# Kernel tuning notes

Measured on AMD Instinct MI355X. Metric: run time of the kernel, lower is better.

The kernel has to match this reference:

```python
import jax, jax.numpy as jnp
import numpy as np


def _iterative_pinv(mat, n_iter=6):
    # mat: [b, h, m, m]
    m = mat.shape[-1]
    I = jnp.eye(m, dtype=mat.dtype)
    # global (over all batch/heads) scaling, matching torch.max over full tensor
    init_coef = jnp.max(jnp.sum(jnp.abs(mat), axis=-2)) * jnp.max(jnp.sum(jnp.abs(mat), axis=-1))
    out = jnp.swapaxes(mat, -2, -1) / init_coef
    for _ in range(n_iter):
        mo = jnp.matmul(mat, out)          # [b,h,m,m]
        term1 = 7.0 * I - mo
        term2 = 15.0 * I - jnp.matmul(mo, term1)
        term3 = 13.0 * I - jnp.matmul(mo, term2)
        out = 0.25 * jnp.matmul(out, term3)
    return out


def _landmarks(x, m):
    # x: [b, h, s, d] -> segment means [b, h, m, d]
    b, h, s, d = x.shape
    l = s // m
    return x.reshape(b, h, m, l, d).mean(axis=-2)


def setup_inputs() -> dict:
    key = jax.random.key(0)
    kq, kk, kv = jax.random.split(key, 3)
    shape = (4, 12, 4096, 64)
    return {
        "query": jax.random.normal(kq, shape, dtype=jnp.float32),
        "key": jax.random.normal(kk, shape, dtype=jnp.float32),
        "value": jax.random.normal(kv, shape, dtype=jnp.float32),
        "num_landmarks": 64,
    }


def reference(query, key, value, num_landmarks):
    b, h, s, d = query.shape
    scale = 1.0 / jnp.sqrt(jnp.asarray(d, dtype=query.dtype))
    q_lm = _landmarks(query, num_landmarks)   # [b,h,m,d]
    k_lm = _landmarks(key, num_landmarks)     # [b,h,m,d]
    # F_tilde: [b,h,s,m]
    F_tilde = jax.nn.softmax(jnp.einsum('bhsd,bhmd->bhsm', query, k_lm) * scale, axis=-1)
    # A_tilde: pinv of [b,h,m,m]
    A_tilde = _iterative_pinv(
        jax.nn.softmax(jnp.einsum('bhnd,bhmd->bhnm', q_lm, k_lm) * scale, axis=-1))
    # B_tilde: [b,h,m,s]
    B_tilde = jax.nn.softmax(jnp.einsum('bhmd,bhsd->bhms', q_lm, key) * scale, axis=-1)
    # out = F_tilde @ (A_tilde @ (B_tilde @ value))  -> [b,h,s,d]
    bv = jnp.matmul(B_tilde, value)        # [b,h,m,d]
    abv = jnp.matmul(A_tilde, bv)          # [b,h,m,d]
    return jnp.matmul(F_tilde, abv)        # [b,h,s,d]
```

## Files before the change

### kernel.cpp

```cpp
#include <hip/hip_runtime.h>
#include <math.h>

#define BH 48
#define Ss 4096
#define Dd 64
#define Mm 64
#define NCH 16
#define SCALE 0.125f
#define PLN 4096

typedef unsigned int u32;
typedef unsigned short u16;
typedef __attribute__((ext_vector_type(8))) short short8;
typedef __attribute__((ext_vector_type(4))) float floatx4;

union FRAG { uint4 u; short8 s; };

#define MFMA(a,b,c) __builtin_amdgcn_mfma_f32_16x16x32_bf16(a,b,c,0,0,0)

__device__ __forceinline__ u32 pack2_hi(float a, float b) {
    return (__float_as_uint(a) >> 16) | (__float_as_uint(b) & 0xFFFF0000u);
}
__device__ __forceinline__ float trunc_bf(float a) {
    return __uint_as_float(__float_as_uint(a) & 0xFFFF0000u);
}
__device__ __forceinline__ void split1(float v, u16& h, u16& l) {
    u32 u = __float_as_uint(v);
    h = (u16)(u >> 16);
    float r = v - __uint_as_float(u & 0xFFFF0000u);
    l = (u16)(__float_as_uint(r) >> 16);
}
__device__ __forceinline__ void split8(const float* v, short8& h, short8& l) {
    FRAG H, L;
    float r[8];
#pragma unroll
    for (int i = 0; i < 8; i++) r[i] = v[i] - trunc_bf(v[i]);
    H.u.x = pack2_hi(v[0], v[1]); H.u.y = pack2_hi(v[2], v[3]);
    H.u.z = pack2_hi(v[4], v[5]); H.u.w = pack2_hi(v[6], v[7]);
    L.u.x = pack2_hi(r[0], r[1]); L.u.y = pack2_hi(r[2], r[3]);
    L.u.z = pack2_hi(r[4], r[5]); L.u.w = pack2_hi(r[6], r[7]);
    h = H.s; l = L.s;
}
__device__ __forceinline__ int swz(int row, int col) {
    return row * 64 + ((((col >> 3) ^ (row & 7)) << 3) | (col & 7));
}

__global__ __launch_bounds__(256) void k_landmarks(const float* __restrict__ Q,
                                                   const float* __restrict__ Kg,
                                                   float* __restrict__ qlm,
                                                   float* __restrict__ klm,
                                                   u16* __restrict__ qlmh, u16* __restrict__ qlml,
                                                   u16* __restrict__ klmh, u16* __restrict__ klml) {
    int g = blockIdx.x, bh = blockIdx.y;
    int t = threadIdx.x;
    int m8 = t >> 5, r5 = t & 31, half = r5 >> 4, d4 = r5 & 15;
    int m = g * 8 + m8;
    __shared__ float4 part[8][16];
    const float* src = blockIdx.z ? Kg : Q;
    float* dst = blockIdx.z ? klm : qlm;
    u16* dh = blockIdx.z ? klmh : qlmh;
    u16* dl = blockIdx.z ? klml : qlml;
    const float* base = src + ((size_t)bh * Ss + (size_t)m * 64 + half * 32) * Dd + d4 * 4;
    float4 acc = make_float4(0.f, 0.f, 0.f, 0.f);
#pragma unroll
    for (int l = 0; l < 32; l++) {
        float4 v = *(const float4*)(base + (size_t)l * Dd);
        acc.x += v.x; acc.y += v.y; acc.z += v.z; acc.w += v.w;
    }
    if (half) part[m8][d4] = acc;
    __syncthreads();
    if (!half) {
        float4 o = part[m8][d4];
        acc.x = (acc.x + o.x) * (1.f / 64.f);
        acc.y = (acc.y + o.y) * (1.f / 64.f);
        acc.z = (acc.z + o.z) * (1.f / 64.f);
        acc.w = (acc.w + o.w) * (1.f / 64.f);
        int idx = (bh * Mm + m) * Dd + d4 * 4;
        *(float4*)(dst + idx) = acc;
        float vv[4] = {acc.x, acc.y, acc.z, acc.w};
        u16 hh[4], ll[4];
#pragma unroll
        for (int i = 0; i < 4; i++) split1(vv[i], hh[i], ll[i]);
        *(uint2*)(dh + idx) = make_uint2((u32)hh[0] | ((u32)hh[1] << 16), (u32)hh[2] | ((u32)hh[3] << 16));
        *(uint2*)(dl + idx) = make_uint2((u32)ll[0] | ((u32)ll[1] << 16), (u32)ll[2] | ((u32)ll[3] << 16));
    }
}

__global__ __launch_bounds__(256) void k_lmsm(const float* __restrict__ qlm,
                                              const float* __restrict__ klm,
                                              float* __restrict__ smat,
                                              unsigned int* __restrict__ coef) {
    int bh = blockIdx.x, t = threadIdx.x;
    __shared__ float kl[Mm * Dd];
    __shared__ float ql[Mm * Dd];
    __shared__ float Lp[Mm][Mm + 1];
    const float4* kb = (const float4*)(klm + bh * Mm * Dd);
    const float4* qb = (const float4*)(qlm + bh * Mm * Dd);
    for (int i = t; i < Mm * Dd / 4; i += 256) {
        ((float4*)kl)[i] = kb[i];
        ((float4*)ql)[i] = qb[i];
    }
    __syncthreads();
    int n = t >> 2, c = t & 3;
    float p[16];
#pragma unroll
    for (int jj = 0; jj < 16; jj++) {
        int m = c * 16 + jj;
        float s = 0.f;
#pragma unroll
        for (int d4 = 0; d4 < 16; d4++) {
            int d = (((d4 + c * 4) & 15)) * 4;
            float4 kv = *(const float4*)(kl + m * Dd + d);
            float4 qv = *(const float4*)(ql + n * Dd + d);
            s += qv.x * kv.x + qv.y * kv.y + qv.z * kv.z + qv.w * kv.w;
        }
        p[jj] = s * SCALE;
    }
    float mx = -INFINITY;
#pragma unroll
    for (int jj = 0; jj < 16; jj++) mx = fmaxf(mx, p[jj]);
    mx = fmaxf(mx, __shfl_xor(mx, 1));
    mx = fmaxf(mx, __shfl_xor(mx, 2));
    float den = 0.f;
#pragma unroll
    for (int jj = 0; jj < 16; jj++) { p[jj] = __expf(p[jj] - mx); den += p[jj]; }
    den += __shfl_xor(den, 1);
    den += __shfl_xor(den, 2);
    float inv = 1.0f / den;
#pragma unroll
    for (int jj = 0; jj < 16; jj++) Lp[n][c * 16 + jj] = p[jj] * inv;
    __syncthreads();
    float* sg = smat + bh * Mm * Mm;
    for (int i = t; i < Mm * Mm; i += 256) sg[i] = Lp[i >> 6][i & 63];
    if (t < Mm) {
        float cs = 0.f;
#pragma unroll
        for (int nn = 0; nn < Mm; nn++) cs += Lp[nn][t];
#pragma unroll
        for (int off = 1; off < 64; off <<= 1) cs = fmaxf(cs, __shfl_xor(cs, off));
        if (t == 0) atomicMax(coef + 0, __float_as_uint(cs));
    } else if (t < 2 * Mm) {
        int nn = t - Mm; float rs = 0.f;
#pragma unroll
        for (int m = 0; m < Mm; m++) rs += Lp[nn][m];
#pragma unroll
        for (int off = 1; off < 64; off <<= 1) rs = fmaxf(rs, __shfl_xor(rs, off));
        if (t == Mm) atomicMax(coef + 1, __float_as_uint(rs));
    }
}

__device__ __forceinline__ void pinv_pass(const u16* __restrict__ Ah, const u16* __restrict__ Al,
                                          const u16* __restrict__ Bph, const u16* __restrict__ Bpl,
                                          u16* __restrict__ Oh, u16* __restrict__ Ol,
                                          int w, int c, int hi,
                                          float diag, float sgn, float scl) {
    short8 bfh[2], bfl[2];
#pragma unroll
    for (int ks = 0; ks < 2; ks++) {
        bfh[ks] = *(const short8*)&Bph[swz(w * 16 + c, ks * 32 + hi * 8)];
        bfl[ks] = *(const short8*)&Bpl[swz(w * 16 + c, ks * 32 + hi * 8)];
    }
    int j = w * 16 + c;
#pragma unroll
    for (int ta = 0; ta < 4; ta++) {
        floatx4 acc = (floatx4){0.f, 0.f, 0.f, 0.f};
#pragma unroll
        for (int ks = 0; ks < 2; ks++) {
            short8 afh = *(const short8*)&Ah[swz(ta * 16 + c, ks * 32 + hi * 8)];
            short8 afl = *(const short8*)&Al[swz(ta * 16 + c, ks * 32 + hi * 8)];
            acc = MFMA(afh, bfh[ks], acc);
            acc = MFMA(afl, bfh[ks], acc);
            acc = MFMA(afh, bfl[ks], acc);
        }
        u16 oh[4], ol[4];
#pragma unroll
        for (int r = 0; r < 4; r++) {
            int i = ta * 16 + hi * 4 + r;
            float v = scl * (((i == j) ? diag : 0.f) + sgn * acc[r]);
            split1(v, oh[r], ol[r]);
        }
        int o0 = swz(j, ta * 16 + hi * 4);
        *(u32*)&Oh[o0]     = (u32)oh[0] | ((u32)oh[1] << 16);
        *(u32*)&Oh[o0 + 2] = (u32)oh[2] | ((u32)oh[3] << 16);
        *(u32*)&Ol[o0]     = (u32)ol[0] | ((u32)ol[1] << 16);
        *(u32*)&Ol[o0 + 2] = (u32)ol[2] | ((u32)ol[3] << 16);
    }
}

__global__ __launch_bounds__(256) void k_pinv(const float* __restrict__ smat,
                                              const unsigned int* __restrict__ coef,
                                              float* __restrict__ atil) {
    extern __shared__ u16 P[];
    u16* FaH  = P;             u16* FaL  = P + PLN;
    u16* FxcH = P + 2 * PLN;   u16* FxcL = P + 3 * PLN;
    u16* X0H  = P + 4 * PLN;   u16* X0L  = P + 5 * PLN;
    u16* X1H  = P + 6 * PLN;   u16* X1L  = P + 7 * PLN;
    u16* T1H  = P + 8 * PLN;   u16* T1L  = P + 9 * PLN;
    u16* T2H  = P + 10 * PLN;  u16* T2L  = P + 11 * PLN;
    int bh = blockIdx.x, t = threadIdx.x;
    int w = t >> 6, l = t & 63, c = l & 15, hi = l >> 4;
    float inv = 1.0f / (__uint_as_float(coef[0]) * __uint_as_float(coef[1]));
    {
        int r = t >> 2, kq = (t & 3) * 16;
        const float* ar = smat + bh * 4096 + r * 64 + kq;
        float v[16];
#pragma unroll
        for (int q = 0; q < 4; q++) {
            float4 x = *(const float4*)(ar + q * 4);
            v[q * 4 + 0] = x.x; v[q * 4 + 1] = x.y; v[q * 4 + 2] = x.z; v[q * 4 + 3] = x.w;
        }
        short8 h0, l0, h1, l1;
        split8(v, h0, l0); split8(v + 8, h1, l1);
        *(short8*)&FaH[swz(r, kq)] = h0;     *(short8*)&FaH[swz(r, kq + 8)] = h1;
        *(short8*)&FaL[swz(r, kq)] = l0;     *(short8*)&FaL[swz(r, kq + 8)] = l1;
        float vs[16];
#pragma unroll
        for (int q = 0; q < 16; q++) vs[q] = v[q] * inv;
        split8(vs, h0, l0); split8(vs + 8, h1, l1);
        *(short8*)&FxcH[swz(r, kq)] = h0;    *(short8*)&FxcH[swz(r, kq + 8)] = h1;
        *(short8*)&FxcL[swz(r, kq)] = l0;    *(short8*)&FxcL[swz(r, kq + 8)] = l1;
#pragma unroll
        for (int q = 0; q < 16; q++) {
            u16 h, lo; split1(vs[q], h, lo);
            X0H[swz(kq + q, r)] = h;
            X0L[swz(kq + q, r)] = lo;
        }
    }
    __syncthreads();
    u16 *xrH = X0H, *xrL = X0L, *moH = X1H, *moL = X1L;
    for (int it = 0; it < 6; it++) {
        pinv_pass(FxcH, FxcL, FaH, FaL, moH, moL, w, c, hi, 0.f, 1.f, 1.f);
        pinv_pass(FaH, FaL, FxcH, FxcL, T1H, T1L, w, c, hi, 7.f, -1.f, 1.f);
        __syncthreads();
        pinv_pass(moH, moL, T1H, T1L, T2H, T2L, w, c, hi, 15.f, -1.f, 1.f);
        __syncthreads();
        pinv_pass(moH, moL, T2H, T2L, T1H, T1L, w, c, hi, 13.f, -1.f, 1.f);
        __syncthreads();
        pinv_pass(T1H, T1L, xrH, xrL, moH, moL, w, c, hi, 0.f, 1.f, 0.25f);
        pinv_pass(xrH, xrL, T1H, T1L, FxcH, FxcL, w, c, hi, 0.f, 1.f, 0.25f);
        __syncthreads();
        u16* th = xrH; xrH = moH; moH = th;
        u16* tl = xrL; xrL = moL; moL = tl;
    }
    {
        int i = t >> 2, j0 = (t & 3) * 16;
        FRAG h0, l0, h1, l1;
        h0.s = *(const short8*)&xrH[swz(i, j0)];
        l0.s = *(const short8*)&xrL[swz(i, j0)];
        h1.s = *(const short8*)&xrH[swz(i, j0 + 8)];
        l1.s = *(const short8*)&xrL[swz(i, j0 + 8)];
        float* ob = atil + bh * 4096 + i * 64 + j0;
#pragma unroll
        for (int q = 0; q < 8; q++) {
            ob[q]     = __uint_as_float(((u32)(u16)h0.s[q]) << 16) + __uint_as_float(((u32)(u16)l0.s[q]) << 16);
            ob[q + 8] = __uint_as_float(((u32)(u16)h1.s[q]) << 16) + __uint_as_float(((u32)(u16)l1.s[q]) << 16);
        }
    }
}

__global__ __launch_bounds__(256) void k_bvp(const float* __restrict__ Kg,
                                             const float* __restrict__ Vg,
                                             const u16* __restrict__ qlmh,
                                             const u16* __restrict__ qlml,
                                             float* __restrict__ pnum,
                                             float* __restrict__ pden) {
    __shared__ __align__(16) u16 Pb[2][4096];
    __shared__ __align__(16) u16 vt[2][4096];
    __shared__ __align__(16) float tmp[64 * 68];
    int ch = blockIdx.x, bh = blockIdx.y;
    int t = threadIdx.x, w = t >> 6, l = t & 63, c = l & 15, hi = l >> 4;
    const float* Kbh = Kg + (size_t)bh * Ss * Dd;
    const float* Vbh = Vg + (size_t)bh * Ss * Dd;
    const u16* qh = qlmh + bh * Mm * Dd;
    const u16* ql = qlml + bh * Mm * Dd;
    floatx4 pvC[4];
    float denacc[16];
#pragma unroll
    for (int i = 0; i < 4; i++) pvC[i] = (floatx4){0.f, 0.f, 0.f, 0.f};
#pragma unroll
    for (int i = 0; i < 16; i++) denacc[i] = 0.f;

    for (int tile = 0; tile < 4; ++tile) {
        int s0 = ch * 256 + tile * 64;
        __syncthreads();
        {
            int sl = t >> 2, q = (t & 3) * 16;
            const float4* vp = (const float4*)(Vbh + (size_t)(s0 + sl) * Dd + q);
            float4* dp = (float4*)(tmp + sl * 68 + q);
#pragma unroll
            for (int qq = 0; qq < 4; qq++) dp[qq] = vp[qq];
        }
        {
            int srow = s0 + w * 16 + c;
            const float* kp = Kbh + (size_t)srow * Dd + hi * 8;
            short8 kbh[2], kbl[2];
#pragma unroll
            for (int ks = 0; ks < 2; ks++) {
                float kv[8];
                float4 a = *(const float4*)(kp + ks * 32);
                float4 b = *(const float4*)(kp + ks * 32 + 4);
                kv[0] = a.x; kv[1] = a.y; kv[2] = a.z; kv[3] = a.w;
                kv[4] = b.x; kv[5] = b.y; kv[6] = b.z; kv[7] = b.w;
                split8(kv, kbh[ks], kbl[ks]);
            }
            floatx4 qkC[4];
#pragma unroll
            for (int i = 0; i < 4; i++) qkC[i] = (floatx4){0.f, 0.f, 0.f, 0.f};
#pragma unroll
            for (int mt = 0; mt < 4; mt++) {
#pragma unroll
                for (int ks = 0; ks < 2; ks++) {
                    short8 aH = *(const short8*)&qh[(mt * 16 + c) * 64 + ks * 32 + hi * 8];
                    short8 aL = *(const short8*)&ql[(mt * 16 + c) * 64 + ks * 32 + hi * 8];
                    qkC[mt] = MFMA(aH, kbh[ks], qkC[mt]);
                    qkC[mt] = MFMA(aL, kbh[ks], qkC[mt]);
                    qkC[mt] = MFMA(aH, kbl[ks], qkC[mt]);
                }
            }
#pragma unroll
            for (int mt = 0; mt < 4; mt++) {
#pragma unroll
                for (int r = 0; r < 4; r++) {
                    float pv = __expf(qkC[mt][r] * SCALE);
                    denacc[mt * 4 + r] += pv;
                    int m = mt * 16 + hi * 4 + r;
                    u16 h, lo; split1(pv, h, lo);
                    Pb[0][swz(m, w * 16 + c)] = h;
                    Pb[1][swz(m, w * 16 + c)] = lo;
                }
            }
        }
        __syncthreads();
        {
            int d = t >> 2, sg = t & 3;
            float v[16];
#pragma unroll
            for (int j = 0; j < 16; j++) v[j] = tmp[(sg * 16 + j) * 68 + d];
            short8 h0, l0, h1, l1;
            split8(v, h0, l0); split8(v + 8, h1, l1);
            *(short8*)&vt[0][swz(d, sg * 16)] = h0;
            *(short8*)&vt[0][swz(d, sg * 16 + 8)] = h1;
            *(short8*)&vt[1][swz(d, sg * 16)] = l0;
            *(short8*)&vt[1][swz(d, sg * 16 + 8)] = l1;
        }
        __syncthreads();
#pragma unroll
        for (int ks = 0; ks < 2; ks++) {
            short8 pah = *(const short8*)&Pb[0][swz(w * 16 + c, ks * 32 + hi * 8)];
            short8 pal = *(const short8*)&Pb[1][swz(w * 16 + c, ks * 32 + hi * 8)];
#pragma unroll
            for (int dt = 0; dt < 4; dt++) {
                short8 vh = *(const short8*)&vt[0][swz(dt * 16 + c, ks * 32 + hi * 8)];
                short8 vl = *(const short8*)&vt[1][swz(dt * 16 + c, ks * 32 + hi * 8)];
                pvC[dt] = MFMA(pah, vh, pvC[dt]);
                pvC[dt] = MFMA(pal, vh, pvC[dt]);
                pvC[dt] = MFMA(pah, vl, pvC[dt]);
            }
        }
    }
    float* nb = pnum + (size_t)(bh * NCH + ch) * 4096;
#pragma unroll
    for (int dt = 0; dt < 4; dt++)
#pragma unroll
        for (int r = 0; r < 4; r++)
            nb[(w * 16 + hi * 4 + r) * 64 + dt * 16 + c] = pvC[dt][r];
#pragma unroll
    for (int i = 0; i < 16; i++) {
        float v = denacc[i];
        v += __shfl_xor(v, 1); v += __shfl_xor(v, 2);
        v += __shfl_xor(v, 4); v += __shfl_xor(v, 8);
        denacc[i] = v;
    }
    if (c == 0) {
        float* db = pden + (size_t)((bh * NCH + ch) * 4 + w) * 64;
#pragma unroll
        for (int mt = 0; mt < 4; mt++)
#pragma unroll
            for (int r = 0; r < 4; r++)
                db[mt * 16 + hi * 4 + r] = denacc[mt * 4 + r];
    }
}

__global__ __launch_bounds__(256) void k_bvc(const float* __restrict__ pnum,
                                             const float* __restrict__ pden,
                                             const float* __restrict__ atil,
                                             u16* __restrict__ abvh,
                                             u16* __restrict__ abvl) {
    int bh = blockIdx.x, t = threadIdx.x;
    __shared__ float bvs[Mm][Dd + 1];
    __shared__ float Ams[Mm * (Mm + 1)];
    const float* ab = atil + bh * Mm * Mm;
    for (int i = t; i < Mm * Mm; i += 256) Ams[(i >> 6) * 65 + (i & 63)] = ab[i];
    int m = t >> 2, c = t & 3, d0 = c * 16;
    float den = 0.f;
    const float* db = pden + (size_t)bh * NCH * 4 * 64;
#pragma unroll
    for (int i = 0; i < NCH * 4; i++) den += db[i * 64 + m];
    float acc[16];
#pragma unroll
    for (int i = 0; i < 16; i++) acc[i] = 0.f;
    const float* nb = pnum + (size_t)bh * NCH * 4096;
    for (int ch = 0; ch < NCH; ch++) {
        const float4* pa = (const float4*)(nb + ch * 4096 + m * 64 + d0);
#pragma unroll
        for (int q = 0; q < 4; q++) {
            float4 v = pa[q];
            acc[q * 4 + 0] += v.x; acc[q * 4 + 1] += v.y;
            acc[q * 4 + 2] += v.z; acc[q * 4 + 3] += v.w;
        }
    }
    float inv = 1.0f / den;
#pragma unroll
    for (int ii = 0; ii < 16; ii++) bvs[m][d0 + ii] = acc[ii] * inv;
    __syncthreads();
    int j = t & 63, i0 = (t >> 6) << 4;
    float outv[16];
#pragma unroll
    for (int ii = 0; ii < 16; ii++) outv[ii] = 0.f;
#pragma unroll
    for (int k = 0; k < Mm; k++) {
        float bk = bvs[k][j];
#pragma unroll
        for (int ii = 0; ii < 16; ii++) outv[ii] += Ams[(i0 + ii) * 65 + k] * bk;
    }
    u16* oh = abvh + bh * 4096;
    u16* ol = abvl + bh * 4096;
#pragma unroll
    for (int ii = 0; ii < 16; ii++) {
        u16 h, lo; split1(outv[ii], h, lo);
        oh[j * 64 + i0 + ii] = h;
        ol[j * 64 + i0 + ii] = lo;
    }
}

__global__ __launch_bounds__(256) void k_fout(const float* __restrict__ Qg,
                                              const u16* __restrict__ klmh,
                                              const u16* __restrict__ klml,
                                              const u16* __restrict__ abvh,
                                              const u16* __restrict__ abvl,
                                              float* __restrict__ Og) {
    __shared__ __align__(16) u16 skh[4096], skl[4096], sah[4096], sal[4096];
    __shared__ __align__(16) u16 Pw[4][2][1024];
    int sb = blockIdx.x, bh = blockIdx.y;
    int t = threadIdx.x, w = t >> 6, l = t & 63, c = l & 15, hi = l >> 4;
    {
        const uint4* s1 = (const uint4*)(klmh + bh * 4096);
        const uint4* s2 = (const uint4*)(klml + bh * 4096);
        const uint4* s3 = (const uint4*)(abvh + bh * 4096);
        const uint4* s4 = (const uint4*)(abvl + bh * 4096);
#pragma unroll
        for (int i0 = 0; i0 < 512; i0 += 256) {
            int i = i0 + t;
            int row = i >> 3, chk = i & 7;
            int d = row * 8 + (chk ^ (row & 7));
            ((uint4*)skh)[d] = s1[i];
            ((uint4*)skl)[d] = s2[i];
            ((uint4*)sah)[d] = s3[i];
            ((uint4*)sal)[d] = s4[i];
        }
    }
    const float* qbase = Qg + ((size_t)bh * Ss + (size_t)sb * 256 + w * 16 + c) * Dd + hi * 8;
    float4 qv0[4];
    qv0[0] = *(const float4*)(qbase + 0);
    qv0[1] = *(const float4*)(qbase + 4);
    qv0[2] = *(const float4*)(qbase + 32);
    qv0[3] = *(const float4*)(qbase + 36);
    __syncthreads();
#pragma unroll
    for (int ti = 0; ti < 4; ti++) {
        float4 qn[4];
        if (ti < 3) {
            const float* q2 = qbase + (ti + 1) * 64 * Dd;
            qn[0] = *(const float4*)(q2 + 0);
            qn[1] = *(const float4*)(q2 + 4);
            qn[2] = *(const float4*)(q2 + 32);
            qn[3] = *(const float4*)(q2 + 36);
        }
        short8 qah[2], qal[2];
        {
            float qq[8];
            qq[0] = qv0[0].x; qq[1] = qv0[0].y; qq[2] = qv0[0].z; qq[3] = qv0[0].w;
            qq[4] = qv0[1].x; qq[5] = qv0[1].y; qq[6] = qv0[1].z; qq[7] = qv0[1].w;
            split8(qq, qah[0], qal[0]);
            qq[0] = qv0[2].x; qq[1] = qv0[2].y; qq[2] = qv0[2].z; qq[3] = qv0[2].w;
            qq[4] = qv0[3].x; qq[5] = qv0[3].y; qq[6] = qv0[3].z; qq[7] = qv0[3].w;
            split8(qq, qah[1], qal[1]);
        }
        floatx4 qkC[4];
#pragma unroll
        for (int i = 0; i < 4; i++) qkC[i] = (floatx4){0.f, 0.f, 0.f, 0.f};
        __builtin_amdgcn_s_setprio(1);
#pragma unroll
        for (int mt = 0; mt < 4; mt++) {
#pragma unroll
            for (int ks = 0; ks < 2; ks++) {
                short8 bH = *(const short8*)&skh[swz(mt * 16 + c, ks * 32 + hi * 8)];
                short8 bL = *(const short8*)&skl[swz(mt * 16 + c, ks * 32 + hi * 8)];
                qkC[mt] = MFMA(qah[ks], bH, qkC[mt]);
                qkC[mt] = MFMA(qal[ks], bH, qkC[mt]);
                qkC[mt] = MFMA(qah[ks], bL, qkC[mt]);
            }
        }
        __builtin_amdgcn_s_setprio(0);
        float p[16], dsum[4];
#pragma unroll
        for (int r = 0; r < 4; r++) dsum[r] = 0.f;
#pragma unroll
        for (int mt = 0; mt < 4; mt++)
#pragma unroll
            for (int r = 0; r < 4; r++) {
                float pv = __expf(qkC[mt][r] * SCALE);
                p[mt * 4 + r] = pv;
                dsum[r] += pv;
            }
#pragma unroll
        for (int r = 0; r < 4; r++) {
            float v = dsum[r];
            v += __shfl_xor(v, 1); v += __shfl_xor(v, 2);
            v += __shfl_xor(v, 4); v += __shfl_xor(v, 8);
            dsum[r] = 1.0f / v;
        }
#pragma unroll
        for (int mt = 0; mt < 4; mt++)
#pragma unroll
            for (int r = 0; r < 4; r++) {
                float pv = p[mt * 4 + r] * dsum[r];
                u16 h, lo; split1(pv, h, lo);
                Pw[w][0][swz(hi * 4 + r, mt * 16 + c)] = h;
                Pw[w][1][swz(hi * 4 + r, mt * 16 + c)] = lo;
            }
        asm volatile("s_waitcnt lgkmcnt(0)" ::: "memory");
        __builtin_amdgcn_sched_barrier(0);
        short8 pah[2], pal[2];
#pragma unroll
        for (int ks = 0; ks < 2; ks++) {
            pah[ks] = *(const short8*)&Pw[w][0][swz(c, ks * 32 + hi * 8)];
            pal[ks] = *(const short8*)&Pw[w][1][swz(c, ks * 32 + hi * 8)];
        }
        floatx4 oC[4];
#pragma unroll
        for (int i = 0; i < 4; i++) oC[i] = (floatx4){0.f, 0.f, 0.f, 0.f};
        __builtin_amdgcn_s_setprio(1);
#pragma unroll
        for (int dt = 0; dt < 4; dt++) {
#pragma unroll
            for (int ks = 0; ks < 2; ks++) {
                short8 bH = *(const short8*)&sah[swz(dt * 16 + c, ks * 32 + hi * 8)];
                short8 bL = *(const short8*)&sal[swz(dt * 16 + c, ks * 32 + hi * 8)];
                oC[dt] = MFMA(pah[ks], bH, oC[dt]);
                oC[dt] = MFMA(pal[ks], bH, oC[dt]);
                oC[dt] = MFMA(pah[ks], bL, oC[dt]);
            }
        }
        __builtin_amdgcn_s_setprio(0);
        float* ob = Og + ((size_t)bh * Ss + (size_t)sb * 256 + ti * 64 + w * 16) * Dd;
#pragma unroll
        for (int dt = 0; dt < 4; dt++)
#pragma unroll
            for (int r = 0; r < 4; r++)
                ob[(hi * 4 + r) * 64 + dt * 16 + c] = oC[dt][r];
        qv0[0] = qn[0]; qv0[1] = qn[1]; qv0[2] = qn[2]; qv0[3] = qn[3];
    }
}

extern "C" void kernel_launch(void* const* d_in, const int* in_sizes, int n_in,
                              void* d_out, int out_size, void* d_ws, size_t ws_size,
                              hipStream_t stream) {
    const float* Q = (const float*)d_in[0];
    const float* K = (const float*)d_in[1];
    const float* V = (const float*)d_in[2];
    float* out = (float*)d_out;
    float* ws = (float*)d_ws;
    unsigned int* coef = (unsigned int*)d_ws;
    float* qlm  = ws + 16;
    float* klm  = qlm  + BH * Mm * Dd;
    float* smat = klm  + BH * Mm * Dd;
    float* atil = smat + BH * Mm * Mm;
    float* pnum = atil + BH * Mm * Mm;
    float* pden = pnum + (size_t)BH * NCH * Mm * Dd;
    u16* ub   = (u16*)(pden + (size_t)BH * NCH * 4 * 64);
    u16* qlmh = ub;
    u16* qlml = qlmh + BH * Mm * Dd;
    u16* klmh = qlml + BH * Mm * Dd;
    u16* klml = klmh + BH * Mm * Dd;
    u16* abvh = klml + BH * Mm * Dd;
    u16* abvl = abvh + BH * Mm * Dd;

    hipMemsetAsync(d_ws, 0, 64, stream);

    k_landmarks<<<dim3(8, BH, 2), dim3(256), 0, stream>>>(Q, K, qlm, klm, qlmh, qlml, klmh, klml);
    k_lmsm<<<dim3(BH), dim3(256), 0, stream>>>(qlm, klm, smat, coef);
    k_pinv<<<dim3(BH), dim3(256), 12 * PLN * 2, stream>>>(smat, coef, atil);
    k_bvp<<<dim3(NCH, BH), dim3(256), 0, stream>>>(K, V, qlmh, qlml, pnum, pden);
    k_bvc<<<dim3(BH), dim3(256), 0, stream>>>(pnum, pden, atil, abvh, abvl);
    k_fout<<<dim3(Ss / 256, BH), dim3(256), 0, stream>>>(Q, klmh, klml, abvh, abvl, out);
}
```

Before: 148.1 us.

## Prefetch next K/V tile in k_bvp with async global-to-LDS loads

The K·V partial-sum kernel is restructured to software-pipeline its tile loop. The next V tile is fetched straight into shared memory with global_load_lds, and the next K fragment is loaded into registers while the current tile is computed. Some full __syncthreads are replaced with lgkmcnt-only barriers, and setprio is raised around the MFMA blocks. The goal is to hide global load latency behind matrix work. In exchange, the padding on the V staging buffer is dropped, which may add LDS bank conflicts during the transpose read, and correctness depends on the ordering of the async loads.

```diff
diff --git a/kernel.cpp b/kernel.cpp
--- a/kernel.cpp
+++ b/kernel.cpp
@@ -17,6 +17,16 @@
 union FRAG { uint4 u; short8 s; };
 
 #define MFMA(a,b,c) __builtin_amdgcn_mfma_f32_16x16x32_bf16(a,b,c,0,0,0)
+
+#define GLOAD_LDS(g, l) __builtin_amdgcn_global_load_lds( \
+    (const __attribute__((address_space(1))) u32*)(g), \
+    (__attribute__((address_space(3))) u32*)(l), 16, 0, 0)
+
+__device__ __forceinline__ void lgkm_barrier() {
+    asm volatile("s_waitcnt lgkmcnt(0)" ::: "memory");
+    __builtin_amdgcn_sched_barrier(0);
+    __builtin_amdgcn_s_barrier();
+}
 
 __device__ __forceinline__ u32 pack2_hi(float a, float b) {
     return (__float_as_uint(a) >> 16) | (__float_as_uint(b) & 0xFFFF0000u);
@@ -266,7 +276,7 @@
                                              float* __restrict__ pden) {
     __shared__ __align__(16) u16 Pb[2][4096];
     __shared__ __align__(16) u16 vt[2][4096];
-    __shared__ __align__(16) float tmp[64 * 68];
+    __shared__ __align__(16) float tmp[4096];
     int ch = blockIdx.x, bh = blockIdx.y;
     int t = threadIdx.x, w = t >> 6, l = t & 63, c = l & 15, hi = l >> 4;
     const float* Kbh = Kg + (size_t)bh * Ss * Dd;
@@ -279,63 +289,78 @@
     for (int i = 0; i < 4; i++) pvC[i] = (floatx4){0.f, 0.f, 0.f, 0.f};
 #pragma unroll
     for (int i = 0; i < 16; i++) denacc[i] = 0.f;
-
+    const float* kp0 = Kbh + (size_t)(ch * 256 + w * 16 + c) * Dd + hi * 8;
+    const float* vsrc0 = Vbh + (size_t)(ch * 256 + w * 16) * Dd
+                       + ((l >> 4) * Dd + (l & 15) * 4);
+#pragma unroll
+    for (int i = 0; i < 4; i++)
+        GLOAD_LDS(vsrc0 + i * 4 * Dd, &tmp[(w * 16 + i * 4) * 64]);
+    float4 kc0 = *(const float4*)(kp0 + 0);
+    float4 kc1 = *(const float4*)(kp0 + 4);
+    float4 kc2 = *(const float4*)(kp0 + 32);
+    float4 kc3 = *(const float4*)(kp0 + 36);
+    float4 kn0, kn1, kn2, kn3;
+#pragma unroll
     for (int tile = 0; tile < 4; ++tile) {
-        int s0 = ch * 256 + tile * 64;
+        short8 kbh[2], kbl[2];
+        {
+            float kq[8];
+            kq[0] = kc0.x; kq[1] = kc0.y; kq[2] = kc0.z; kq[3] = kc0.w;
+            kq[4] = kc1.x; kq[5] = kc1.y; kq[6] = kc1.z; kq[7] = kc1.w;
+            split8(kq, kbh[0], kbl[0]);
+            kq[0] = kc2.x; kq[1] = kc2.y; kq[2] = kc2.z; kq[3] = kc2.w;
+            kq[4] = kc3.x; kq[5] = kc3.y; kq[6] = kc3.z; kq[7] = kc3.w;
+            split8(kq, kbh[1], kbl[1]);
+        }
+        floatx4 qkC[4];
+#pragma unroll
+        for (int i = 0; i < 4; i++) qkC[i] = (floatx4){0.f, 0.f, 0.f, 0.f};
+        __builtin_amdgcn_s_setprio(1);
+#pragma unroll
+        for (int mt = 0; mt < 4; mt++) {
+#pragma unroll
+            for (int ks = 0; ks < 2; ks++) {
+                short8 aH = *(const short8*)&qh[(mt * 16 + c) * 64 + ks * 32 + hi * 8];
+                short8 aL = *(const short8*)&ql[(mt * 16 + c) * 64 + ks * 32 + hi * 8];
+                qkC[mt] = MFMA(aH, kbh[ks], qkC[mt]);
+                qkC[mt] = MFMA(aL, kbh[ks], qkC[mt]);
+                qkC[mt] = MFMA(aH, kbl[ks], qkC[mt]);
+            }
+        }
+        __builtin_amdgcn_s_setprio(0);
+#pragma unroll
+        for (int mt = 0; mt < 4; mt++) {
+#pragma unroll
+            for (int r = 0; r < 4; r++) {
+                float pv = __expf(qkC[mt][r] * SCALE);
+                denacc[mt * 4 + r] += pv;
+                int m = mt * 16 + hi * 4 + r;
+                u16 h, lo; split1(pv, h, lo);
+                Pb[0][swz(m, w * 16 + c)] = h;
+                Pb[1][swz(m, w * 16 + c)] = lo;
+            }
+        }
         __syncthreads();
-        {
-            int sl = t >> 2, q = (t & 3) * 16;
-            const float4* vp = (const float4*)(Vbh + (size_t)(s0 + sl) * Dd + q);
-            float4* dp = (float4*)(tmp + sl * 68 + q);
-#pragma unroll
-            for (int qq = 0; qq < 4; qq++) dp[qq] = vp[qq];
-        }
-        {
-            int srow = s0 + w * 16 + c;
-            const float* kp = Kbh + (size_t)srow * Dd + hi * 8;
-            short8 kbh[2], kbl[2];
-#pragma unroll
-            for (int ks = 0; ks < 2; ks++) {
-                float kv[8];
-                float4 a = *(const float4*)(kp + ks * 32);
-                float4 b = *(const float4*)(kp + ks * 32 + 4);
-                kv[0] = a.x; kv[1] = a.y; kv[2] = a.z; kv[3] = a.w;
-                kv[4] = b.x; kv[5] = b.y; kv[6] = b.z; kv[7] = b.w;
-                split8(kv, kbh[ks], kbl[ks]);
-            }
-            floatx4 qkC[4];
-#pragma unroll
-            for (int i = 0; i < 4; i++) qkC[i] = (floatx4){0.f, 0.f, 0.f, 0.f};
-#pragma unroll
-            for (int mt = 0; mt < 4; mt++) {
-#pragma unroll
-                for (int ks = 0; ks < 2; ks++) {
-                    short8 aH = *(const short8*)&qh[(mt * 16 + c) * 64 + ks * 32 + hi * 8];
-                    short8 aL = *(const short8*)&ql[(mt * 16 + c) * 64 + ks * 32 + hi * 8];
-                    qkC[mt] = MFMA(aH, kbh[ks], qkC[mt]);
-                    qkC[mt] = MFMA(aL, kbh[ks], qkC[mt]);
-                    qkC[mt] = MFMA(aH, kbl[ks], qkC[mt]);
-                }
-            }
-#pragma unroll
-            for (int mt = 0; mt < 4; mt++) {
-#pragma unroll
-                for (int r = 0; r < 4; r++) {
-                    float pv = __expf(qkC[mt][r] * SCALE);
-                    denacc[mt * 4 + r] += pv;
-                    int m = mt * 16 + hi * 4 + r;
-                    u16 h, lo; split1(pv, h, lo);
-                    Pb[0][swz(m, w * 16 + c)] = h;
-                    Pb[1][swz(m, w * 16 + c)] = lo;
-                }
-            }
-        }
-        __syncthreads();
+        float v[16];
         {
             int d = t >> 2, sg = t & 3;
-            float v[16];
-#pragma unroll
-            for (int j = 0; j < 16; j++) v[j] = tmp[(sg * 16 + j) * 68 + d];
+#pragma unroll
+            for (int j = 0; j < 16; j++) v[j] = tmp[(sg * 16 + j) * 64 + d];
+        }
+        lgkm_barrier();
+        if (tile < 3) {
+            const float* vs = vsrc0 + (size_t)(tile + 1) * 64 * Dd;
+#pragma unroll
+            for (int i = 0; i < 4; i++)
+                GLOAD_LDS(vs + i * 4 * Dd, &tmp[(w * 16 + i * 4) * 64]);
+            const float* kp = kp0 + (size_t)(tile + 1) * 64 * Dd;
+            kn0 = *(const float4*)(kp + 0);
+            kn1 = *(const float4*)(kp + 4);
+            kn2 = *(const float4*)(kp + 32);
+            kn3 = *(const float4*)(kp + 36);
+        }
+        {
+            int d = t >> 2, sg = t & 3;
             short8 h0, l0, h1, l1;
             split8(v, h0, l0); split8(v + 8, h1, l1);
             *(short8*)&vt[0][swz(d, sg * 16)] = h0;
@@ -343,7 +368,8 @@
             *(short8*)&vt[1][swz(d, sg * 16)] = l0;
             *(short8*)&vt[1][swz(d, sg * 16 + 8)] = l1;
         }
-        __syncthreads();
+        lgkm_barrier();
+        __builtin_amdgcn_s_setprio(1);
 #pragma unroll
         for (int ks = 0; ks < 2; ks++) {
             short8 pah = *(const short8*)&Pb[0][swz(w * 16 + c, ks * 32 + hi * 8)];
@@ -357,6 +383,9 @@
                 pvC[dt] = MFMA(pah, vl, pvC[dt]);
             }
         }
+        __builtin_amdgcn_s_setprio(0);
+        lgkm_barrier();
+        kc0 = kn0; kc1 = kn1; kc2 = kn2; kc3 = kn3;
     }
     float* nb = pnum + (size_t)(bh * NCH + ch) * 4096;
 #pragma unroll
```

New measurement: 163.6 us. 10.5% more time.
